# Kernel optimization log

Measured on AMD Instinct MI355X. Metric: run time of the kernel, lower is better.

The kernel has to match this reference:

```python
import jax, jax.numpy as jnp
import numpy as np

CUTOFF = 15.0
EPS = 1e-08


def _pairwise_dist(x):
    # x: [B, N, 3] -> [B, N, N] euclidean distances (gram trick, no [B,N,N,3] temp)
    x2 = jnp.sum(x * x, axis=-1)                      # [B, N]
    d2 = x2[:, :, None] + x2[:, None, :] - 2.0 * jnp.einsum('bnd,bmd->bnm', x, x)
    d2 = jnp.maximum(d2, 0.0)
    return jnp.sqrt(d2)


def setup_inputs() -> dict:
    key = jax.random.key(0)
    k1, k2 = jax.random.split(key)
    B, N = 8, 2048
    pred_coords = jax.random.normal(k1, (B, N, 3), dtype=jnp.float32)
    true_coords = jax.random.normal(k2, (B, N, 3), dtype=jnp.float32)
    return {"pred_coords": pred_coords, "true_coords": true_coords}


def reference(pred_coords, true_coords):
    pred_d = _pairwise_dist(pred_coords)              # [B, N, N]
    true_d = _pairwise_dist(true_coords)              # [B, N, N]
    local_mask = (true_d < CUTOFF) & (true_d > EPS)   # excludes diagonal
    diff = jnp.abs(pred_d - true_d)
    # piecewise-constant preserved score (0.5/1.0/2.0/4.0 A bins)
    preserved = (
        (diff < 0.5).astype(jnp.float32) * 1.0
        + ((diff >= 0.5) & (diff < 1.0)).astype(jnp.float32) * 0.5
        + ((diff >= 1.0) & (diff < 2.0)).astype(jnp.float32) * 0.25
        + ((diff >= 2.0) & (diff < 4.0)).astype(jnp.float32) * 0.125
    )
    maskf = local_mask.astype(jnp.float32)
    numerator = jnp.sum(preserved * maskf, axis=(-1, -2))    # [B]
    denominator = jnp.maximum(jnp.sum(maskf, axis=(-1, -2)), EPS)
    lddt_per_sample = numerator / denominator
    return jnp.mean(1.0 - lddt_per_sample)
```

## Files before the change

kernel.cpp:

```cpp
#include <hip/hip_runtime.h>
#include <math.h>

constexpr int B  = 8;
constexpr int N  = 2048;
constexpr int TI = 256;
constexpr int TJ = 64;
constexpr int TILES = 144;


template <bool CHECK>
__device__ __forceinline__ void inner_loop(
    const float4* __restrict__ sj,
    float pix, float piy, float piz,
    float tix, float tiy, float tiz,
    int j0, int i,
    unsigned& c0, unsigned& c1, unsigned& c2, unsigned& c3, unsigned& cd)
{
    #pragma unroll 8
    for (int j = 0; j < TJ; ++j) {
        float4 p4 = sj[2 * j + 0];
        float4 t4 = sj[2 * j + 1];

        float dx = pix - p4.x, dy = piy - p4.y, dz = piz - p4.z;
        float pd2 = fmaf(dx, dx, fmaf(dy, dy, dz * dz));
        float ex = tix - t4.x, ey = tiy - t4.y, ez = tiz - t4.z;
        float td2 = fmaf(ex, ex, fmaf(ey, ey, ez * ez));

        unsigned long long m = __ballot(td2 < 225.0f);
        if (CHECK) m &= __ballot(j0 + j > i);

        float diff = fabsf(__builtin_amdgcn_sqrtf(pd2) - __builtin_amdgcn_sqrtf(td2));

        c0 += __popcll(m & __ballot(diff < 0.5f));
        c1 += __popcll(m & __ballot(diff < 1.0f));
        c2 += __popcll(m & __ballot(diff < 2.0f));
        c3 += __popcll(m & __ballot(diff < 4.0f));
        cd += __popcll(m);
    }
}

__global__ __launch_bounds__(TI) void lddt_partial(
    const float* __restrict__ pred,
    const float* __restrict__ truec,
    float* __restrict__ part)
{
    const int b = blockIdx.y;
    int r = blockIdx.x, a = 0;
    while (r >= 32 - 4 * a) { r -= 32 - 4 * a; ++a; }
    const int c = 4 * a + r;
    const int i0 = a * TI;
    const int j0 = c * TJ;
    const int t = threadIdx.x;

    __shared__ float4 sj[TJ * 2];

    if (t < TJ) {
        const float* pp = pred  + ((size_t)b * N + j0 + t) * 3;
        const float* tp = truec + ((size_t)b * N + j0 + t) * 3;
        sj[2 * t + 0] = make_float4(pp[0], pp[1], pp[2], 0.0f);
        sj[2 * t + 1] = make_float4(tp[0], tp[1], tp[2], 0.0f);
    }

    const int i = i0 + t;
    const float* pi = pred  + ((size_t)b * N + i) * 3;
    const float* ti = truec + ((size_t)b * N + i) * 3;
    const float pix = pi[0], piy = pi[1], piz = pi[2];
    const float tix = ti[0], tiy = ti[1], tiz = ti[2];
    __syncthreads();

    unsigned c0 = 0, c1 = 0, c2 = 0, c3 = 0, cd = 0;

    if (c >= 4 * a + 4) {
        inner_loop<false>(sj, pix, piy, piz, tix, tiy, tiz, j0, i, c0, c1, c2, c3, cd);
    } else {
        inner_loop<true>(sj, pix, piy, piz, tix, tiy, tiz, j0, i, c0, c1, c2, c3, cd);
    }

    __shared__ float rnum[TI / 64];
    __shared__ float rden[TI / 64];
    const int wave = t >> 6;
    const int lane = t & 63;
    if (lane == 0) {
        rnum[wave] = 0.5f * (float)c0 + 0.25f * (float)c1
                   + 0.125f * (float)c2 + 0.125f * (float)c3;
        rden[wave] = (float)cd;
    }
    __syncthreads();

    if (t == 0) {
        float n = 0.0f, d = 0.0f;
        #pragma unroll
        for (int w = 0; w < TI / 64; ++w) { n += rnum[w]; d += rden[w]; }
        float* slot = part + ((size_t)b * TILES + blockIdx.x) * 2;
        slot[0] = n;
        slot[1] = d;
    }
}

__global__ __launch_bounds__(512) void lddt_reduce(
    const float* __restrict__ part,
    float* __restrict__ out)
{
    const int t = threadIdx.x;
    const int w = t >> 6;
    const int l = t & 63;

    float n = 0.0f, d = 0.0f;
    for (int s = l; s < TILES; s += 64) {
        const float* slot = part + ((size_t)w * TILES + s) * 2;
        n += slot[0];
        d += slot[1];
    }
    for (int off = 32; off > 0; off >>= 1) {
        n += __shfl_down(n, off, 64);
        d += __shfl_down(d, off, 64);
    }

    __shared__ float acc[B];
    if (l == 0) acc[w] = 1.0f - n / fmaxf(d, 1e-8f);
    __syncthreads();

    if (t == 0) {
        float s = 0.0f;
        #pragma unroll
        for (int b = 0; b < B; ++b) s += acc[b];
        out[0] = s / (float)B;
    }
}

extern "C" void kernel_launch(void* const* d_in, const int* in_sizes, int n_in,
                              void* d_out, int out_size, void* d_ws, size_t ws_size,
                              hipStream_t stream)
{
    const float* pred  = (const float*)d_in[0];
    const float* truec = (const float*)d_in[1];
    float* out  = (float*)d_out;
    float* part = (float*)d_ws;

    dim3 grid(TILES, B);
    lddt_partial<<<grid, TI, 0, stream>>>(pred, truec, part);
    lddt_reduce<<<1, 512, 0, stream>>>(part, out);
}
```

Baseline: 71.30 us.

## Replace ballot counting with per-lane counters and read j-points directly from global

Each lane now counts its own threshold hits with a masked sentinel compare, where before every comparison went through a wave-wide ballot plus popcount. The counts are summed by a shuffle reduction once, after the loop. The LDS staging of j coordinates and its barrier are removed, so the j coordinates become wave-uniform loads straight from global memory, which the compiler may turn into scalar loads. The aim is to cut the per-pair ballot, SALU and LDS traffic, in exchange for reliance on cached global loads and a slightly longer reduction at the end.

```diff
diff --git a/kernel.cpp b/kernel.cpp
--- a/kernel.cpp
+++ b/kernel.cpp
@@ -7,10 +7,10 @@
 constexpr int TJ = 64;
 constexpr int TILES = 144;
 
-
 template <bool CHECK>
 __device__ __forceinline__ void inner_loop(
-    const float4* __restrict__ sj,
+    const float* __restrict__ pj,
+    const float* __restrict__ tj,
     float pix, float piy, float piz,
     float tix, float tiy, float tiz,
     int j0, int i,
@@ -18,24 +18,25 @@
 {
     #pragma unroll 8
     for (int j = 0; j < TJ; ++j) {
-        float4 p4 = sj[2 * j + 0];
-        float4 t4 = sj[2 * j + 1];
+        float jx = pj[3 * j + 0], jy = pj[3 * j + 1], jz = pj[3 * j + 2];
+        float ux = tj[3 * j + 0], uy = tj[3 * j + 1], uz = tj[3 * j + 2];
 
-        float dx = pix - p4.x, dy = piy - p4.y, dz = piz - p4.z;
+        float dx = pix - jx, dy = piy - jy, dz = piz - jz;
         float pd2 = fmaf(dx, dx, fmaf(dy, dy, dz * dz));
-        float ex = tix - t4.x, ey = tiy - t4.y, ez = tiz - t4.z;
+        float ex = tix - ux, ey = tiy - uy, ez = tiz - uz;
         float td2 = fmaf(ex, ex, fmaf(ey, ey, ez * ez));
 
-        unsigned long long m = __ballot(td2 < 225.0f);
-        if (CHECK) m &= __ballot(j0 + j > i);
+        bool m = td2 < 225.0f;
+        if (CHECK) m = m && (j0 + j > i);
 
         float diff = fabsf(__builtin_amdgcn_sqrtf(pd2) - __builtin_amdgcn_sqrtf(td2));
+        float de = m ? diff : 3.0e38f;
 
-        c0 += __popcll(m & __ballot(diff < 0.5f));
-        c1 += __popcll(m & __ballot(diff < 1.0f));
-        c2 += __popcll(m & __ballot(diff < 2.0f));
-        c3 += __popcll(m & __ballot(diff < 4.0f));
-        cd += __popcll(m);
+        c0 += (de < 0.5f);
+        c1 += (de < 1.0f);
+        c2 += (de < 2.0f);
+        c3 += (de < 4.0f);
+        cd += m;
     }
 }
 
@@ -52,48 +53,46 @@
     const int j0 = c * TJ;
     const int t = threadIdx.x;
 
-    __shared__ float4 sj[TJ * 2];
-
-    if (t < TJ) {
-        const float* pp = pred  + ((size_t)b * N + j0 + t) * 3;
-        const float* tp = truec + ((size_t)b * N + j0 + t) * 3;
-        sj[2 * t + 0] = make_float4(pp[0], pp[1], pp[2], 0.0f);
-        sj[2 * t + 1] = make_float4(tp[0], tp[1], tp[2], 0.0f);
-    }
+    const float* pj = pred  + ((size_t)b * N + j0) * 3;
+    const float* tj = truec + ((size_t)b * N + j0) * 3;
 
     const int i = i0 + t;
     const float* pi = pred  + ((size_t)b * N + i) * 3;
     const float* ti = truec + ((size_t)b * N + i) * 3;
     const float pix = pi[0], piy = pi[1], piz = pi[2];
     const float tix = ti[0], tiy = ti[1], tiz = ti[2];
-    __syncthreads();
 
     unsigned c0 = 0, c1 = 0, c2 = 0, c3 = 0, cd = 0;
 
     if (c >= 4 * a + 4) {
-        inner_loop<false>(sj, pix, piy, piz, tix, tiy, tiz, j0, i, c0, c1, c2, c3, cd);
+        inner_loop<false>(pj, tj, pix, piy, piz, tix, tiy, tiz, j0, i, c0, c1, c2, c3, cd);
     } else {
-        inner_loop<true>(sj, pix, piy, piz, tix, tiy, tiz, j0, i, c0, c1, c2, c3, cd);
+        inner_loop<true>(pj, tj, pix, piy, piz, tix, tiy, tiz, j0, i, c0, c1, c2, c3, cd);
+    }
+
+    float n = 0.5f * (float)c0 + 0.25f * (float)c1
+            + 0.125f * (float)c2 + 0.125f * (float)c3;
+    float d = (float)cd;
+    #pragma unroll
+    for (int off = 32; off > 0; off >>= 1) {
+        n += __shfl_down(n, off, 64);
+        d += __shfl_down(d, off, 64);
     }
 
     __shared__ float rnum[TI / 64];
     __shared__ float rden[TI / 64];
     const int wave = t >> 6;
     const int lane = t & 63;
-    if (lane == 0) {
-        rnum[wave] = 0.5f * (float)c0 + 0.25f * (float)c1
-                   + 0.125f * (float)c2 + 0.125f * (float)c3;
-        rden[wave] = (float)cd;
-    }
+    if (lane == 0) { rnum[wave] = n; rden[wave] = d; }
     __syncthreads();
 
     if (t == 0) {
-        float n = 0.0f, d = 0.0f;
+        float nn = 0.0f, dd = 0.0f;
         #pragma unroll
-        for (int w = 0; w < TI / 64; ++w) { n += rnum[w]; d += rden[w]; }
+        for (int w = 0; w < TI / 64; ++w) { nn += rnum[w]; dd += rden[w]; }
         float* slot = part + ((size_t)b * TILES + blockIdx.x) * 2;
-        slot[0] = n;
-        slot[1] = d;
+        slot[0] = nn;
+        slot[1] = dd;
     }
 }
 
```

Measured after the change: 74.49 us. +4.5%, slower.

## Broadcast j coords via readlane and skip waves below diagonal

Applied to the files above, without the earlier changes.

Replaces LDS staging of the j-tile with per-lane register loads broadcast through readlane, removing shared memory use and a barrier. In diagonal blocks, waves whose rows lie entirely below the diagonal now skip computation, and the triangle mask becomes lane-relative. readlane adds scalar/VALU dependency traffic per pair, which could cost more than LDS broadcast reads.

```diff
diff --git a/kernel.cpp b/kernel.cpp
--- a/kernel.cpp
+++ b/kernel.cpp
@@ -7,27 +7,31 @@
 constexpr int TJ = 64;
 constexpr int TILES = 144;
 
+__device__ __forceinline__ float rlane(float v, int l) {
+    return __uint_as_float(__builtin_amdgcn_readlane(__float_as_uint(v), l));
+}
 
 template <bool CHECK>
 __device__ __forceinline__ void inner_loop(
-    const float4* __restrict__ sj,
+    float vjx, float vjy, float vjz,
+    float vux, float vuy, float vuz,
     float pix, float piy, float piz,
     float tix, float tiy, float tiz,
-    int j0, int i,
+    int lane,
     unsigned& c0, unsigned& c1, unsigned& c2, unsigned& c3, unsigned& cd)
 {
-    #pragma unroll 8
-    for (int j = 0; j < TJ; ++j) {
-        float4 p4 = sj[2 * j + 0];
-        float4 t4 = sj[2 * j + 1];
+    #pragma unroll 16
+    for (int jj = 0; jj < TJ; ++jj) {
+        float jx = rlane(vjx, jj), jy = rlane(vjy, jj), jz = rlane(vjz, jj);
+        float ux = rlane(vux, jj), uy = rlane(vuy, jj), uz = rlane(vuz, jj);
 
-        float dx = pix - p4.x, dy = piy - p4.y, dz = piz - p4.z;
+        float dx = pix - jx, dy = piy - jy, dz = piz - jz;
         float pd2 = fmaf(dx, dx, fmaf(dy, dy, dz * dz));
-        float ex = tix - t4.x, ey = tiy - t4.y, ez = tiz - t4.z;
+        float ex = tix - ux, ey = tiy - uy, ez = tiz - uz;
         float td2 = fmaf(ex, ex, fmaf(ey, ey, ez * ez));
 
         unsigned long long m = __ballot(td2 < 225.0f);
-        if (CHECK) m &= __ballot(j0 + j > i);
+        if (CHECK) m &= __ballot(jj > lane);
 
         float diff = fabsf(__builtin_amdgcn_sqrtf(pd2) - __builtin_amdgcn_sqrtf(td2));
 
@@ -47,50 +51,50 @@
     const int b = blockIdx.y;
     int r = blockIdx.x, a = 0;
     while (r >= 32 - 4 * a) { r -= 32 - 4 * a; ++a; }
-    const int c = 4 * a + r;
+    const int k = r;
     const int i0 = a * TI;
-    const int j0 = c * TJ;
+    const int j0 = (4 * a + k) * TJ;
     const int t = threadIdx.x;
-
-    __shared__ float4 sj[TJ * 2];
-
-    if (t < TJ) {
-        const float* pp = pred  + ((size_t)b * N + j0 + t) * 3;
-        const float* tp = truec + ((size_t)b * N + j0 + t) * 3;
-        sj[2 * t + 0] = make_float4(pp[0], pp[1], pp[2], 0.0f);
-        sj[2 * t + 1] = make_float4(tp[0], tp[1], tp[2], 0.0f);
-    }
-
-    const int i = i0 + t;
-    const float* pi = pred  + ((size_t)b * N + i) * 3;
-    const float* ti = truec + ((size_t)b * N + i) * 3;
-    const float pix = pi[0], piy = pi[1], piz = pi[2];
-    const float tix = ti[0], tiy = ti[1], tiz = ti[2];
-    __syncthreads();
+    const int w = t >> 6;
+    const int lane = t & 63;
 
     unsigned c0 = 0, c1 = 0, c2 = 0, c3 = 0, cd = 0;
 
-    if (c >= 4 * a + 4) {
-        inner_loop<false>(sj, pix, piy, piz, tix, tiy, tiz, j0, i, c0, c1, c2, c3, cd);
-    } else {
-        inner_loop<true>(sj, pix, piy, piz, tix, tiy, tiz, j0, i, c0, c1, c2, c3, cd);
+    if (k >= w) {
+        const int i = i0 + t;
+        const float* pi = pred  + ((size_t)b * N + i) * 3;
+        const float* ti = truec + ((size_t)b * N + i) * 3;
+        const float pix = pi[0], piy = pi[1], piz = pi[2];
+        const float tix = ti[0], tiy = ti[1], tiz = ti[2];
+
+        const float* pj = pred  + ((size_t)b * N + j0 + lane) * 3;
+        const float* tj = truec + ((size_t)b * N + j0 + lane) * 3;
+        const float vjx = pj[0], vjy = pj[1], vjz = pj[2];
+        const float vux = tj[0], vuy = tj[1], vuz = tj[2];
+
+        if (k > w) {
+            inner_loop<false>(vjx, vjy, vjz, vux, vuy, vuz,
+                              pix, piy, piz, tix, tiy, tiz, lane,
+                              c0, c1, c2, c3, cd);
+        } else {
+            inner_loop<true>(vjx, vjy, vjz, vux, vuy, vuz,
+                             pix, piy, piz, tix, tiy, tiz, lane,
+                             c0, c1, c2, c3, cd);
+        }
     }
 
     __shared__ float rnum[TI / 64];
     __shared__ float rden[TI / 64];
-    const int wave = t >> 6;
-    const int lane = t & 63;
     if (lane == 0) {
-        rnum[wave] = 0.5f * (float)c0 + 0.25f * (float)c1
-                   + 0.125f * (float)c2 + 0.125f * (float)c3;
-        rden[wave] = (float)cd;
+        rnum[w] = 0.125f * (float)(4u * c0 + 2u * c1 + c2 + c3);
+        rden[w] = (float)cd;
     }
     __syncthreads();
 
     if (t == 0) {
         float n = 0.0f, d = 0.0f;
         #pragma unroll
-        for (int w = 0; w < TI / 64; ++w) { n += rnum[w]; d += rden[w]; }
+        for (int q = 0; q < TI / 64; ++q) { n += rnum[q]; d += rden[q]; }
         float* slot = part + ((size_t)b * TILES + blockIdx.x) * 2;
         slot[0] = n;
         slot[1] = d;
```

Measured after the change: 77.95 us. 9.3% more time.
